# Optimization experiments

Hardware: AMD Instinct MI355X
Metric: run time of the kernel (lower is better)

The kernel has to match this reference:

```python
import jax, jax.numpy as jnp
import numpy as np

B, N, D_IN, H, F = 2, 2048, 512, 8, 64
NEG_SLOPE = 0.2


def setup_inputs() -> dict:
    key = jax.random.key(0)
    k0, k1, k2, k3 = jax.random.split(key, 4)
    nodes = jax.random.normal(k0, (B, N, D_IN), dtype=jnp.float32)
    edges = jax.random.randint(k1, (B, N, N, 1), 0, 2).astype(jnp.int32)
    # ensure every node has at least one neighbor (self-loop) so softmax is finite
    idx = jnp.arange(N)
    edges = edges.at[:, idx, idx, :].set(1)
    W = jax.random.normal(k2, (D_IN, H * F), dtype=jnp.float32) * 0.02
    a = jax.random.normal(k3, (2 * F,), dtype=jnp.float32) * 0.02
    return {"nodes": nodes, "edges": edges, "W": W, "a": a}


def reference(nodes, edges, W, a):
    b, n, _ = nodes.shape
    mapped = (nodes @ W).reshape(b, n, H, F)  # [B,N,H,F]
    # additive attention: attn([m_i ; m_j]) = a_l . m_i + a_r . m_j
    a_l, a_r = a[:F], a[F:]
    el = jnp.einsum('bnhf,f->bnh', mapped, a_l)
    er = jnp.einsum('bnhf,f->bnh', mapped, a_r)
    scores = jax.nn.leaky_relu(el[:, :, None, :] + er[:, None, :, :], negative_slope=NEG_SLOPE)  # [B,N,N,H]
    mask = edges != 0  # [B,N,N,1] broadcasts over heads
    scores = jnp.where(mask, scores, -jnp.inf)
    attn_weights = jax.nn.softmax(scores, axis=2)  # softmax over neighbors j
    attn_res = jnp.einsum('bijh,bjhf->bihf', attn_weights, mapped)  # [B,N,H,F]
    # is_concat=False path: mean over heads, then sigmoid
    return jax.nn.sigmoid(attn_res.mean(axis=2))  # [B,N,F]
```

## Files before the change

### kernel.cpp

```cpp
#include <hip/hip_runtime.h>
#include <hip/hip_bf16.h>
#include <math.h>

#define Bq   2
#define Nq   2048
#define DIN  512
#define Hq   8
#define Fq   64
#define NEG  0.2f

using short8 = __attribute__((ext_vector_type(8))) short;
using f32x4  = __attribute__((ext_vector_type(4))) float;

__device__ inline unsigned int bf16_rne(float x) {
    unsigned int u = __float_as_uint(x);
    u += 0x7fffu + ((u >> 16) & 1u);
    return u >> 16;
}

#define AFRAG_BLOCKS 256
#define WFRAG_BLOCKS 128

__global__ __launch_bounds__(256) void prep_kernel(
    const float* __restrict__ nodes, ushort* __restrict__ Afrag,
    const float* __restrict__ W,     ushort* __restrict__ Wfrag)
{
    __shared__ __align__(16) char smem[16 * 516 * 4];
    const int bid = blockIdx.x;
    const int t   = threadIdx.x;

    if (bid < AFRAG_BLOCKS) {
        float (*As)[516] = (float(*)[516])smem;
        const int mt = bid;
        {
            const int row = t >> 4, c = t & 15;
#pragma unroll
            for (int i = 0; i < 8; i++) {
                float4 v = *(const float4*)&nodes[((size_t)mt * 16 + row) * DIN + (c + i * 16) * 4];
                *(float4*)&As[row][(c + i * 16) * 4] = v;
            }
        }
        __syncthreads();
        const int lane = t & 63, ksg = t >> 6;
        const int quad = lane >> 4, l15 = lane & 15;
#pragma unroll
        for (int k2 = 0; k2 < 4; k2++) {
            int ks = ksg * 4 + k2;
            const float* src = &As[l15][ks * 32 + quad * 8];
            float4 f0 = *(const float4*)src;
            float4 f1 = *(const float4*)(src + 4);
            uint4 pk;
            pk.x = bf16_rne(f0.x) | (bf16_rne(f0.y) << 16);
            pk.y = bf16_rne(f0.z) | (bf16_rne(f0.w) << 16);
            pk.z = bf16_rne(f1.x) | (bf16_rne(f1.y) << 16);
            pk.w = bf16_rne(f1.z) | (bf16_rne(f1.w) << 16);
            *(uint4*)(Afrag + ((size_t)(mt * 16 + ks) * 64 + lane) * 8) = pk;
        }
        return;
    }

    {
        float (*Ws)[68] = (float(*)[68])smem;
        const int id = bid - AFRAG_BLOCKS;
        const int ks = id & 15, h = id >> 4;
        {
            const int row = t >> 3, c = t & 7;
            const float* src = &W[(size_t)(ks * 32 + row) * (Hq * Fq) + h * 64 + c * 8];
            float4 v0 = *(const float4*)src;
            float4 v1 = *(const float4*)(src + 4);
            *(float4*)&Ws[row][c * 8]     = v0;
            *(float4*)&Ws[row][c * 8 + 4] = v1;
        }
        __syncthreads();
        const int lane = t & 63, nf = t >> 6;
        const int quad = lane >> 4, l15 = lane & 15;
        float f[8];
#pragma unroll
        for (int jj = 0; jj < 8; jj++) f[jj] = Ws[quad * 8 + jj][nf * 16 + l15];
        uint4 pk;
        pk.x = bf16_rne(f[0]) | (bf16_rne(f[1]) << 16);
        pk.y = bf16_rne(f[2]) | (bf16_rne(f[3]) << 16);
        pk.z = bf16_rne(f[4]) | (bf16_rne(f[5]) << 16);
        pk.w = bf16_rne(f[6]) | (bf16_rne(f[7]) << 16);
        *(uint4*)(Wfrag + (((size_t)(h * 16 + ks) * 4 + nf) * 64 + lane) * 8) = pk;
    }
}

#define GEMM_BLOCKS 512
#define PACK_BLOCKS 1024

__global__ __launch_bounds__(256) void work_kernel(
    const ushort* __restrict__ Afrag, const ushort* __restrict__ Wfrag,
    const float*  __restrict__ avec,
    ushort* __restrict__ Vfrag,
    float* __restrict__ el_t,
    float* __restrict__ er_t,
    const int* __restrict__ edges, unsigned int* __restrict__ ebT)
{
    const int bid = blockIdx.x;
    const int t   = threadIdx.x;

    if (bid >= GEMM_BLOCKS) {
        int gid = (bid - GEMM_BLOCKS) * 256 + t;
        int i = gid & 2047;
        int w = (gid >> 11) & 63;
        int b = gid >> 17;
        const int4* ep = (const int4*)(edges + (((size_t)b * Nq + i) * Nq + w * 32));
        unsigned int word = 0;
#pragma unroll
        for (int c = 0; c < 8; c++) {
            int4 v = ep[c];
            word |= (v.x != 0 ? 1u : 0u) << (c * 4);
            word |= (v.y != 0 ? 1u : 0u) << (c * 4 + 1);
            word |= (v.z != 0 ? 1u : 0u) << (c * 4 + 2);
            word |= (v.w != 0 ? 1u : 0u) << (c * 4 + 3);
        }
        ebT[((size_t)b * 64 + w) * Nq + i] = word;
        return;
    }

    const int lane = t & 63;
    const int wv   = t >> 6;
    const int quad = lane >> 4;
    const int l15  = lane & 15;
    const int h    = bid >> 6;
    const int mt   = (bid & 63) * 4 + wv;
    const int row0 = mt * 16;

    const ushort* ap = Afrag + (size_t)mt * 8192 + lane * 8;
    const ushort* bp = Wfrag + (size_t)h * 32768 + lane * 8;

    f32x4 zero4 = {0.f, 0.f, 0.f, 0.f};
    f32x4 acc[4] = {zero4, zero4, zero4, zero4};

    short8 a0, a1, b0[4], b1[4];
    a0 = *(const short8*)(ap);
#pragma unroll
    for (int nf = 0; nf < 4; nf++) b0[nf] = *(const short8*)(bp + nf * 512);

    for (int ks = 0; ks < 16; ks += 2) {
        a1 = *(const short8*)(ap + (ks + 1) * 512);
#pragma unroll
        for (int nf = 0; nf < 4; nf++) b1[nf] = *(const short8*)(bp + (ks + 1) * 2048 + nf * 512);
#pragma unroll
        for (int nf = 0; nf < 4; nf++)
            acc[nf] = __builtin_amdgcn_mfma_f32_16x16x32_bf16(a0, b0[nf], acc[nf], 0, 0, 0);
        a0 = *(const short8*)(ap + (ks + 2) * 512);
#pragma unroll
        for (int nf = 0; nf < 4; nf++) b0[nf] = *(const short8*)(bp + (ks + 2) * 2048 + nf * 512);
#pragma unroll
        for (int nf = 0; nf < 4; nf++)
            acc[nf] = __builtin_amdgcn_mfma_f32_16x16x32_bf16(a1, b1[nf], acc[nf], 0, 0, 0);
    }

    float aL[4], aR[4];
#pragma unroll
    for (int nf = 0; nf < 4; nf++) {
        aL[nf] = avec[nf * 16 + l15];
        aR[nf] = avec[Fq + nf * 16 + l15];
    }
    const int bb = row0 >> 11;
    const int bh = bb * Hq + h;
#pragma unroll
    for (int r = 0; r < 4; r++) {
        float pl = acc[0][r] * aL[0] + acc[1][r] * aL[1] + acc[2][r] * aL[2] + acc[3][r] * aL[3];
        float pr = acc[0][r] * aR[0] + acc[1][r] * aR[1] + acc[2][r] * aR[2] + acc[3][r] * aR[3];
#pragma unroll
        for (int off = 1; off < 16; off <<= 1) {
            pl += __shfl_xor(pl, off, 64);
            pr += __shfl_xor(pr, off, 64);
        }
        if (l15 == 0) {
            int n = (row0 + quad * 4 + r) & (Nq - 1);
            el_t[(size_t)bh * Nq + n] = pl;
            er_t[(size_t)bh * Nq + n] = pr;
        }
    }

    const int n_base = row0 & (Nq - 1);
    const int sblk   = n_base >> 5;
    const int quadp  = ((wv & 1) << 1) | (quad >> 1);
    const int jj0    = (quad & 1) * 4;
#pragma unroll
    for (int nf = 0; nf < 4; nf++) {
        unsigned int r0 = bf16_rne(acc[nf][0]), r1 = bf16_rne(acc[nf][1]);
        unsigned int r2 = bf16_rne(acc[nf][2]), r3 = bf16_rne(acc[nf][3]);
        uint2 pk;
        pk.x = r0 | (r1 << 16);
        pk.y = r2 | (r3 << 16);
        size_t off = ((((size_t)bh * 64 + sblk) * 4 + nf) * 64 + quadp * 16 + l15) * 8 + jj0;
        *(uint2*)(Vfrag + off) = pk;
    }
}

__global__ __launch_bounds__(256) void attn_kernel(
    const float* __restrict__ el_t, const float* __restrict__ er_t,
    const ushort* __restrict__ Vfrag,
    const unsigned int* __restrict__ ebT, float* __restrict__ attn)
{
    const int lane = threadIdx.x & 63;
    const int wv   = threadIdx.x >> 6;
    const int quad = lane >> 4;
    const int l15  = lane & 15;
    const int bid  = blockIdx.x;
    const int it   = bid & 31;
    const int h    = (bid >> 5) & 7;
    const int b    = bid >> 8;
    const int bh   = b * Hq + h;
    const int i0   = it * 64 + wv * 16;

    __shared__ float smax[4];
    const float* errow = er_t + (size_t)bh * Nq;
    float mx = -INFINITY;
#pragma unroll
    for (int ii = 0; ii < 8; ii++) mx = fmaxf(mx, errow[threadIdx.x + ii * 256]);
#pragma unroll
    for (int off = 32; off > 0; off >>= 1) mx = fmaxf(mx, __shfl_xor(mx, off, 64));
    if (lane == 0) smax[wv] = mx;
    __syncthreads();
    const float emax = fmaxf(fmaxf(smax[0], smax[1]), fmaxf(smax[2], smax[3]));

    const float elv = el_t[(size_t)bh * Nq + i0 + l15];
    const float xm  = elv + emax;
    const float m0  = fmaxf(xm, NEG * xm);
    const float c1  = elv - m0, c2 = NEG * elv - m0;

    const float*        erp = er_t + (size_t)bh * Nq;
    const ushort*       vp  = Vfrag + (size_t)bh * 131072 + lane * 8;
    const unsigned int* e0p = ebT + (size_t)b * 64 * Nq + i0 + l15;

    f32x4 zero4 = {0.f, 0.f, 0.f, 0.f};
    f32x4 acc[4] = {zero4, zero4, zero4, zero4};
    float l0 = 0.f;

    for (int s = 0; s < 64; s++) {
        short8 vb0 = *(const short8*)(vp + s * 2048);
        short8 vb1 = *(const short8*)(vp + s * 2048 + 512);
        short8 vb2 = *(const short8*)(vp + s * 2048 + 1024);
        short8 vb3 = *(const short8*)(vp + s * 2048 + 1536);
        unsigned int w0 = e0p[(size_t)s * Nq];
        float4 ea  = *(const float4*)(erp + s * 32 + quad * 8);
        float4 ebv = *(const float4*)(erp + s * 32 + quad * 8 + 4);

        const unsigned int wq0 = w0 >> (quad * 8);
        float er8[8] = {ea.x, ea.y, ea.z, ea.w, ebv.x, ebv.y, ebv.z, ebv.w};
        unsigned int u0[8];
#pragma unroll
        for (int jj = 0; jj < 8; jj++) {
            float e  = er8[jj];
            float t0 = fmaxf(e + c1, fmaf(NEG, e, c2));
            float x0 = __expf(t0);
            int k0 = ((int)(wq0 << (31 - jj))) >> 31;
            u0[jj] = __float_as_uint(x0) & (unsigned int)k0;
            l0 += __uint_as_float(u0[jj]);
        }
        union { short8 s8; unsigned int w[4]; } af0;
        af0.w[0] = __builtin_amdgcn_perm(u0[1], u0[0], 0x07060302);
        af0.w[1] = __builtin_amdgcn_perm(u0[3], u0[2], 0x07060302);
        af0.w[2] = __builtin_amdgcn_perm(u0[5], u0[4], 0x07060302);
        af0.w[3] = __builtin_amdgcn_perm(u0[7], u0[6], 0x07060302);

        acc[0] = __builtin_amdgcn_mfma_f32_16x16x32_bf16(af0.s8, vb0, acc[0], 0, 0, 0);
        acc[1] = __builtin_amdgcn_mfma_f32_16x16x32_bf16(af0.s8, vb1, acc[1], 0, 0, 0);
        acc[2] = __builtin_amdgcn_mfma_f32_16x16x32_bf16(af0.s8, vb2, acc[2], 0, 0, 0);
        acc[3] = __builtin_amdgcn_mfma_f32_16x16x32_bf16(af0.s8, vb3, acc[3], 0, 0, 0);
    }

    l0 += __shfl_xor(l0, 16, 64);
    l0 += __shfl_xor(l0, 32, 64);
    float lr[4];
#pragma unroll
    for (int r = 0; r < 4; r++) lr[r] = __shfl(l0, quad * 4 + r, 64);

#pragma unroll
    for (int nf = 0; nf < 4; nf++)
#pragma unroll
        for (int r = 0; r < 4; r++)
            attn[(((size_t)b * Nq + i0 + quad * 4 + r) * Hq + h) * Fq + nf * 16 + l15] =
                acc[nf][r] / lr[r];
}

__global__ __launch_bounds__(256) void out_kernel(
    const float* __restrict__ attn, float* __restrict__ out)
{
    const int idx = blockIdx.x * 256 + threadIdx.x;
    const int f   = idx & 63;
    const int bn  = idx >> 6;
    const float* p = attn + (size_t)bn * Hq * Fq + f;
    float s = 0.f;
#pragma unroll
    for (int h = 0; h < Hq; h++) s += p[h * Fq];
    s *= (1.f / Hq);
    out[idx] = 1.f / (1.f + __expf(-s));
}

extern "C" void kernel_launch(void* const* d_in, const int* in_sizes, int n_in,
                              void* d_out, int out_size, void* d_ws, size_t ws_size,
                              hipStream_t stream) {
    const float* nodes = (const float*)d_in[0];
    const int*   edges = (const int*)d_in[1];
    const float* W     = (const float*)d_in[2];
    const float* a     = (const float*)d_in[3];
    float* out = (float*)d_out;

    char* ws = (char*)d_ws;
    ushort* Afrag = (ushort*)ws;           ws += (size_t)Bq * Nq * DIN * 2;
    ushort* Wfrag = (ushort*)ws;           ws += (size_t)DIN * Hq * Fq * 2;
    ushort* Vfrag = (ushort*)ws;           ws += (size_t)Bq * Hq * Nq * Fq * 2;
    float*  el_t  = (float*)ws;            ws += (size_t)Bq * Hq * Nq * 4;
    float*  er_t  = (float*)ws;            ws += (size_t)Bq * Hq * Nq * 4;
    unsigned int* ebT = (unsigned int*)ws; ws += (size_t)Bq * (Nq / 32) * Nq * 4;
    float*  attn  = (float*)ws;

    prep_kernel<<<AFRAG_BLOCKS + WFRAG_BLOCKS, 256, 0, stream>>>(nodes, Afrag, W, Wfrag);
    work_kernel<<<GEMM_BLOCKS + PACK_BLOCKS, 256, 0, stream>>>(
        Afrag, Wfrag, a, Vfrag, el_t, er_t, edges, ebT);
    attn_kernel<<<Bq * Hq * (Nq / 64), 256, 0, stream>>>(el_t, er_t, Vfrag, ebT, attn);
    out_kernel<<<(Bq * Nq * Fq) / 256, 256, 0, stream>>>(attn, out);
}
```

Before: 131.2 us.

## Split attention neighbor loop across two wave groups and use exp2

The attention kernel now launches 512 threads per block: two groups of four waves each process half of the neighbor blocks (split-K), then combine partial accumulators and row sums through shared memory before normalizing. This doubles the waves available to hide the per-iteration load and exp latency, at the cost of an extra LDS reduction and barrier. Separately, the exponent is folded into base-2 by prescaling constants by log2(e) and calling the hardware exp2 directly, which saves a multiply per element.

```diff
diff --git a/kernel.cpp b/kernel.cpp
--- a/kernel.cpp
+++ b/kernel.cpp
@@ -193,13 +193,15 @@
     }
 }
 
-__global__ __launch_bounds__(256) void attn_kernel(
+__global__ __launch_bounds__(512) void attn_kernel(
     const float* __restrict__ el_t, const float* __restrict__ er_t,
     const ushort* __restrict__ Vfrag,
     const unsigned int* __restrict__ ebT, float* __restrict__ attn)
 {
     const int lane = threadIdx.x & 63;
-    const int wv   = threadIdx.x >> 6;
+    const int wv8  = threadIdx.x >> 6;
+    const int rg   = wv8 & 3;
+    const int kh   = wv8 >> 2;
     const int quad = lane >> 4;
     const int l15  = lane & 15;
     const int bid  = blockIdx.x;
@@ -207,23 +209,27 @@
     const int h    = (bid >> 5) & 7;
     const int b    = bid >> 8;
     const int bh   = b * Hq + h;
-    const int i0   = it * 64 + wv * 16;
-
-    __shared__ float smax[4];
+    const int i0   = it * 64 + rg * 16;
+
+    __shared__ float smax[8];
     const float* errow = er_t + (size_t)bh * Nq;
     float mx = -INFINITY;
 #pragma unroll
-    for (int ii = 0; ii < 8; ii++) mx = fmaxf(mx, errow[threadIdx.x + ii * 256]);
+    for (int ii = 0; ii < 4; ii++) mx = fmaxf(mx, errow[threadIdx.x + ii * 512]);
 #pragma unroll
     for (int off = 32; off > 0; off >>= 1) mx = fmaxf(mx, __shfl_xor(mx, off, 64));
-    if (lane == 0) smax[wv] = mx;
+    if (lane == 0) smax[wv8] = mx;
     __syncthreads();
-    const float emax = fmaxf(fmaxf(smax[0], smax[1]), fmaxf(smax[2], smax[3]));
+    float emax = smax[0];
+#pragma unroll
+    for (int q = 1; q < 8; q++) emax = fmaxf(emax, smax[q]);
 
     const float elv = el_t[(size_t)bh * Nq + i0 + l15];
     const float xm  = elv + emax;
     const float m0  = fmaxf(xm, NEG * xm);
-    const float c1  = elv - m0, c2 = NEG * elv - m0;
+    const float R   = 1.4426950408889634f;
+    const float R2  = NEG * R;
+    const float c1  = (elv - m0) * R, c2 = (NEG * elv - m0) * R;
 
     const float*        erp = er_t + (size_t)bh * Nq;
     const ushort*       vp  = Vfrag + (size_t)bh * 131072 + lane * 8;
@@ -233,7 +239,8 @@
     f32x4 acc[4] = {zero4, zero4, zero4, zero4};
     float l0 = 0.f;
 
-    for (int s = 0; s < 64; s++) {
+    const int s_beg = kh * 32, s_end = kh * 32 + 32;
+    for (int s = s_beg; s < s_end; s++) {
         short8 vb0 = *(const short8*)(vp + s * 2048);
         short8 vb1 = *(const short8*)(vp + s * 2048 + 512);
         short8 vb2 = *(const short8*)(vp + s * 2048 + 1024);
@@ -248,8 +255,8 @@
 #pragma unroll
         for (int jj = 0; jj < 8; jj++) {
             float e  = er8[jj];
-            float t0 = fmaxf(e + c1, fmaf(NEG, e, c2));
-            float x0 = __expf(t0);
+            float t0 = fmaxf(fmaf(R, e, c1), fmaf(R2, e, c2));
+            float x0 = __builtin_amdgcn_exp2f(t0);
             int k0 = ((int)(wq0 << (31 - jj))) >> 31;
             u0[jj] = __float_as_uint(x0) & (unsigned int)k0;
             l0 += __uint_as_float(u0[jj]);
@@ -266,18 +273,37 @@
         acc[3] = __builtin_amdgcn_mfma_f32_16x16x32_bf16(af0.s8, vb3, acc[3], 0, 0, 0);
     }
 
-    l0 += __shfl_xor(l0, 16, 64);
-    l0 += __shfl_xor(l0, 32, 64);
-    float lr[4];
-#pragma unroll
-    for (int r = 0; r < 4; r++) lr[r] = __shfl(l0, quad * 4 + r, 64);
-
-#pragma unroll
-    for (int nf = 0; nf < 4; nf++)
-#pragma unroll
-        for (int r = 0; r < 4; r++)
-            attn[(((size_t)b * Nq + i0 + quad * 4 + r) * Hq + h) * Fq + nf * 16 + l15] =
-                acc[nf][r] / lr[r];
+    __shared__ __align__(16) float lds_acc[4][16][65];
+    __shared__ float lds_l[4][64];
+    if (kh == 1) {
+#pragma unroll
+        for (int nf = 0; nf < 4; nf++)
+#pragma unroll
+            for (int r = 0; r < 4; r++)
+                lds_acc[rg][quad * 4 + r][nf * 16 + l15] = acc[nf][r];
+        lds_l[rg][lane] = l0;
+    }
+    __syncthreads();
+    if (kh == 0) {
+#pragma unroll
+        for (int nf = 0; nf < 4; nf++)
+#pragma unroll
+            for (int r = 0; r < 4; r++)
+                acc[nf][r] += lds_acc[rg][quad * 4 + r][nf * 16 + l15];
+        l0 += lds_l[rg][lane];
+        l0 += __shfl_xor(l0, 16, 64);
+        l0 += __shfl_xor(l0, 32, 64);
+        float lr[4];
+#pragma unroll
+        for (int r = 0; r < 4; r++) lr[r] = __shfl(l0, quad * 4 + r, 64);
+
+#pragma unroll
+        for (int nf = 0; nf < 4; nf++)
+#pragma unroll
+            for (int r = 0; r < 4; r++)
+                attn[(((size_t)b * Nq + i0 + quad * 4 + r) * Hq + h) * Fq + nf * 16 + l15] =
+                    acc[nf][r] / lr[r];
+    }
 }
 
 __global__ __launch_bounds__(256) void out_kernel(
@@ -315,6 +341,6 @@
     prep_kernel<<<AFRAG_BLOCKS + WFRAG_BLOCKS, 256, 0, stream>>>(nodes, Afrag, W, Wfrag);
     work_kernel<<<GEMM_BLOCKS + PACK_BLOCKS, 256, 0, stream>>>(
         Afrag, Wfrag, a, Vfrag, el_t, er_t, edges, ebT);
-    attn_kernel<<<Bq * Hq * (Nq / 64), 256, 0, stream>>>(el_t, er_t, Vfrag, ebT, attn);
+    attn_kernel<<<Bq * Hq * (Nq / 64), 512, 0, stream>>>(el_t, er_t, Vfrag, ebT, attn);
     out_kernel<<<(Bq * Nq * Fq) / 256, 256, 0, stream>>>(attn, out);
 }
```

After: 124.6 us. 1.05x faster.
